# Kernel tuning notes

Measured on AMD Instinct MI355X. Metric: run time of the kernel, lower is better.

## Reference

```python
import jax, jax.numpy as jnp
import numpy as np

DIM = 192; HEADS = 6; HDIM = DIM // HEADS
WS = (2, 8, 8); SS = (1, 4, 4)
B, D, H, W = 2, 8, 64, 64
N = WS[0] * WS[1] * WS[2]          # 128 tokens per window
MLP_H = int(DIM * 2.0)
SCALE = HDIM ** -0.5


def _rel_pos_index_np():
    wd, wh, ww = WS
    coords = np.stack(np.meshgrid(np.arange(wd), np.arange(wh), np.arange(ww), indexing='ij'))
    cf = coords.reshape(3, -1)                      # (3, N)
    rel = (cf[:, :, None] - cf[:, None, :]).transpose(1, 2, 0)  # (N, N, 3)
    rel[..., 0] += wd - 1; rel[..., 1] += wh - 1; rel[..., 2] += ww - 1
    rel[..., 0] *= (2 * wh - 1) * (2 * ww - 1)
    rel[..., 1] *= (2 * ww - 1)
    return rel.sum(-1).astype(np.int32)            # (N, N)


def _compute_mask_np():
    wd, wh, ww = WS; sd, sh, sw = SS
    Dp = -(-D // wd) * wd; Hp = -(-H // wh) * wh; Wp = -(-W // ww) * ww
    img = np.zeros((1, Dp, Hp, Wp, 1), np.float32)
    cnt = 0
    for ds in (slice(0, -wd), slice(-wd, -sd), slice(-sd, None)):
        for hs in (slice(0, -wh), slice(-wh, -sh), slice(-sh, None)):
            for vs in (slice(0, -ww), slice(-ww, -sw), slice(-sw, None)):
                img[:, ds, hs, vs, :] = cnt; cnt += 1
    m = img.reshape(1, Dp // wd, wd, Hp // wh, wh, Wp // ww, ww, 1)
    m = m.transpose(0, 1, 3, 5, 2, 4, 6, 7).reshape(-1, N)       # (nW, N)
    am = m[:, None, :] - m[:, :, None]
    return np.where(am != 0, -100.0, 0.0).astype(np.float32)     # (nW, N, N)


def setup_inputs() -> dict:
    key = jax.random.key(0)
    ks = jax.random.split(key, 6)
    f = lambda k, s: (jax.random.normal(k, s, jnp.float32) * 0.02)
    n_bias = (2 * WS[0] - 1) * (2 * WS[1] - 1) * (2 * WS[2] - 1)  # 675
    return dict(
        x=jax.random.normal(ks[0], (B, D, H, W, DIM), jnp.float32),
        mask_matrix=jnp.asarray(_compute_mask_np()),
        rel_pos_index=jnp.asarray(_rel_pos_index_np()),
        gamma1=jnp.ones((DIM,), jnp.float32), beta1=jnp.zeros((DIM,), jnp.float32),
        w_qkv=f(ks[1], (3 * DIM, DIM)), b_qkv=jnp.zeros((3 * DIM,), jnp.float32),
        rpb=f(ks[2], (n_bias, HEADS)),
        w_proj=f(ks[3], (DIM, DIM)), b_proj=jnp.zeros((DIM,), jnp.float32),
        gamma2=jnp.ones((DIM,), jnp.float32), beta2=jnp.zeros((DIM,), jnp.float32),
        w_fc1=f(ks[4], (MLP_H, DIM)), b_fc1=jnp.zeros((MLP_H,), jnp.float32),
        w_fc2=f(ks[5], (DIM, MLP_H)), b_fc2=jnp.zeros((DIM,), jnp.float32),
    )


def _ln(x, g, b, eps=1e-5):
    mu = x.mean(-1, keepdims=True)
    var = ((x - mu) ** 2).mean(-1, keepdims=True)
    return (x - mu) * jax.lax.rsqrt(var + eps) * g + b


def _stl(x, mask, rpi, gamma1, beta1, w_qkv, b_qkv, rpb, w_proj, b_proj,
         gamma2, beta2, w_fc1, b_fc1, w_fc2, b_fc2):
    wd, wh, ww = WS; sd, sh, sw = SS
    # ---- part1: LN -> pad -> roll -> window attention -> reverse ----
    xn = _ln(x, gamma1, beta1)
    pd = (wd - D % wd) % wd; ph = (wh - H % wh) % wh; pw = (ww - W % ww) % ww
    xn = jnp.pad(xn, ((0, 0), (0, pd), (0, ph), (0, pw), (0, 0)))
    Dp, Hp, Wp = D + pd, H + ph, W + pw
    sx = jnp.roll(xn, (-sd, -sh, -sw), axis=(1, 2, 3))
    # window partition -> (Bw, N, C)
    xw = sx.reshape(B, Dp // wd, wd, Hp // wh, wh, Wp // ww, ww, DIM)
    xw = xw.transpose(0, 1, 3, 5, 2, 4, 6, 7).reshape(-1, N, DIM)
    Bw = xw.shape[0]
    qkv = (xw @ w_qkv.T + b_qkv).reshape(Bw, N, 3, HEADS, HDIM).transpose(2, 0, 3, 1, 4)
    q, k, v = qkv[0] * SCALE, qkv[1], qkv[2]
    attn = jnp.einsum('bhnd,bhmd->bhnm', q, k)
    bias = rpb[rpi.reshape(-1)].reshape(N, N, HEADS).transpose(2, 0, 1)  # (H, N, N)
    attn = attn + bias[None]
    nW = mask.shape[0]
    attn = (attn.reshape(Bw // nW, nW, HEADS, N, N) + mask[None, :, None]).reshape(Bw, HEADS, N, N)
    attn = jax.nn.softmax(attn, axis=-1)
    out = jnp.einsum('bhnm,bhmd->bhnd', attn, v).transpose(0, 2, 1, 3).reshape(Bw, N, DIM)
    out = out @ w_proj.T + b_proj
    # window reverse -> un-roll -> slice
    sx = out.reshape(B, Dp // wd, Hp // wh, Wp // ww, wd, wh, ww, DIM)
    sx = sx.transpose(0, 1, 4, 2, 5, 3, 6, 7).reshape(B, Dp, Hp, Wp, DIM)
    part1 = jnp.roll(sx, (sd, sh, sw), axis=(1, 2, 3))[:, :D, :H, :W, :]
    x = x + part1
    # ---- part2: LN -> MLP (GELU, exact) ----
    y = _ln(x, gamma2, beta2)
    h = jax.nn.gelu(y @ w_fc1.T + b_fc1, approximate=False)
    return x + (h @ w_fc2.T + b_fc2)


def reference(x, mask_matrix, rel_pos_index, gamma1, beta1, w_qkv, b_qkv, rpb,
              w_proj, b_proj, gamma2, beta2, w_fc1, b_fc1, w_fc2, b_fc2):
    return _stl(x, mask_matrix, rel_pos_index, gamma1, beta1, w_qkv, b_qkv, rpb,
                w_proj, b_proj, gamma2, beta2, w_fc1, b_fc1, w_fc2, b_fc2)
```

## Files before the change

### kernel.cpp

```cpp
#include <hip/hip_runtime.h>
#include <hip/hip_bf16.h>
#include <math.h>

#define TOKS   65536
#define DIMC   192
#define NTOK   128
#define MLPH   384
#define QSCALE 0.17677669529663687f

typedef unsigned short u16;
typedef unsigned int   u32;
typedef __attribute__((ext_vector_type(8))) short bf16x8;
typedef __attribute__((ext_vector_type(4))) float f32x4;

static __device__ __forceinline__ float gelu_exact(float v) {
    return 0.5f * v * (1.f + erff(v * 0.70710678118654752f));
}
static __device__ __forceinline__ u16 f2bf(float f) {
    __hip_bfloat16 h = __float2bfloat16(f);
    return *reinterpret_cast<u16*>(&h);
}
static __device__ __forceinline__ float bf2f(u16 b) {
    u32 u = ((u32)b) << 16;
    float f;
    __builtin_memcpy(&f, &u, 4);
    return f;
}
static __device__ __forceinline__ void gl_lds16(const u16* g, u16* l) {
    __builtin_amdgcn_global_load_lds(
        (const __attribute__((address_space(1))) void*)g,
        (__attribute__((address_space(3))) void*)l, 16, 0, 0);
}

#define OFF_XW   0u
#define OFF_Q    6291456u
#define OFF_K    12582912u
#define OFF_V    18874368u
#define OFF_BF   25165824u
#define OFF_WB   25264128u

__global__ __launch_bounds__(256) void k_prep(const float* __restrict__ a,
                                              const float* __restrict__ b,
                                              const float* __restrict__ c,
                                              const float* __restrict__ d,
                                              u16* __restrict__ o,
                                              const float* __restrict__ rpb,
                                              const int* __restrict__ rpi,
                                              u16* __restrict__ biasw) {
    int bid = blockIdx.x;
    if (bid < 1152) {
        int i = bid * 256 + threadIdx.x;
        float v;
        if (i < 110592) v = a[i];
        else if (i < 147456) v = b[i - 110592];
        else if (i < 221184) v = c[i - 147456];
        else v = d[i - 221184];
        o[i] = f2bf(v);
    } else {
        int idx = (bid - 1152) * 256 + threadIdx.x;
        int h = idx >> 14;
        int n = (idx >> 7) & 127;
        int slot = idx & 127;
        int m = ((slot & 7) << 4) + (slot >> 3);
        biasw[idx] = f2bf(rpb[rpi[n * 128 + m] * 6 + h]);
    }
}

template<bool PERMUTE>
__global__ __launch_bounds__(256) void k_ln(const float* __restrict__ x,
                                            const float* __restrict__ gamma,
                                            const float* __restrict__ beta,
                                            u16* __restrict__ out) {
    int tid  = threadIdx.x;
    int lane = tid & 63, wv = tid >> 6;
    int tk = blockIdx.x * 4 + wv;
    size_t src;
    if (PERMUTE) {
        int w_all = tk >> 7, t = tk & 127;
        int b  = w_all >> 8, rem = w_all & 255;
        int di = rem >> 6, hi = (rem >> 3) & 7, wi = rem & 7;
        int qd = (di * 2 + (t >> 6) + 1) & 7;
        int qh = (hi * 8 + ((t >> 3) & 7) + 4) & 63;
        int qw = (wi * 8 + (t & 7) + 4) & 63;
        src = ((size_t)(((b * 8 + qd) * 64 + qh) * 64 + qw)) * DIMC;
    } else {
        src = (size_t)tk * DIMC;
    }
    float v0 = x[src + lane];
    float v1 = x[src + 64 + lane];
    float v2 = x[src + 128 + lane];
    float s  = v0 + v1 + v2;
    float sq = v0 * v0 + v1 * v1 + v2 * v2;
    #pragma unroll
    for (int off = 32; off; off >>= 1) {
        s  += __shfl_xor(s, off);
        sq += __shfl_xor(sq, off);
    }
    float mu   = s * (1.f / 192.f);
    float var  = sq * (1.f / 192.f) - mu * mu;
    float rstd = rsqrtf(var + 1e-5f);
    size_t o = (size_t)tk * DIMC;
    out[o + lane]       = f2bf((v0 - mu) * rstd * gamma[lane]       + beta[lane]);
    out[o + 64 + lane]  = f2bf((v1 - mu) * rstd * gamma[64 + lane]  + beta[64 + lane]);
    out[o + 128 + lane] = f2bf((v2 - mu) * rstd * gamma[128 + lane] + beta[128 + lane]);
}

template<int MODE, int KD>
__global__ __launch_bounds__(256) void k_mgemm(const u16* __restrict__ A,
                                               const u16* __restrict__ W,
                                               const float* __restrict__ bias,
                                               void* __restrict__ outp,
                                               const float* __restrict__ aux,
                                               u16* __restrict__ q_o,
                                               u16* __restrict__ k_o,
                                               u16* __restrict__ v_o) {
    __shared__ u16 As[2][128 * 64];
    u16*   Eu = (u16*)As;
    float* Ef = (float*)As;
    const int tid = threadIdx.x;
    const int wv = tid >> 6, l = tid & 63;
    const int l15 = l & 15, g4 = l >> 4;
    const int wm = wv >> 1, wn = wv & 1;
    constexpr int NY  = (MODE == 0) ? 9 : (MODE == 2) ? 6 : 3;
    constexpr int CHK = 512 * NY / 8;
    const int bid = blockIdx.x;
    const int logical = (bid & 7) * CHK + (bid >> 3);
    const int xb = logical / NY;
    const int yb = logical - xb * NY;
    const size_t m0 = (size_t)xb * 128;
    const int n0 = yb * 64;
    const int srow = l >> 3, scol = l & 7;
    const int w = (int)(m0 >> 7);

    f32x4 acc[4][2] = {};

    const u16* Wb = W + (size_t)(n0 + wn * 32 + l15) * KD + g4 * 8;
    bf16x8 wfr[3][2][2];
    #pragma unroll
    for (int t = 0; t < 3; ++t)
        #pragma unroll
        for (int kk = 0; kk < 2; ++kk)
            #pragma unroll
            for (int nt = 0; nt < 2; ++nt)
                wfr[t][kk][nt] = *(const bf16x8*)&Wb[(size_t)(nt * 16) * KD + t * 64 + kk * 32];

    auto STAGE = [&](int b, int tcol) {
        const u16* Ab = A + m0 * KD + tcol * 64;
        #pragma unroll
        for (int j = 0; j < 4; ++j) {
            int row = (wv * 4 + j) * 8 + srow;
            int sc  = scol ^ (row & 7);
            gl_lds16(Ab + (size_t)row * KD + sc * 8, &As[b][(wv * 4 + j) * 512]);
        }
    };
    auto COMPUTE = [&](int b, int t) {
        #pragma unroll
        for (int kk = 0; kk < 2; ++kk) {
            bf16x8 bfr[2];
            if (t < 3) {
                bfr[0] = wfr[t][kk][0];
                bfr[1] = wfr[t][kk][1];
            } else {
                #pragma unroll
                for (int nt = 0; nt < 2; ++nt)
                    bfr[nt] = *(const bf16x8*)&Wb[(size_t)(nt * 16) * KD + t * 64 + kk * 32];
            }
            #pragma unroll
            for (int mt = 0; mt < 4; ++mt) {
                int row  = wm * 64 + mt * 16 + l15;
                int slot = (kk * 4 + g4) ^ (row & 7);
                bf16x8 afr = *(const bf16x8*)&As[b][row * 64 + slot * 8];
                #pragma unroll
                for (int nt = 0; nt < 2; ++nt)
                    acc[mt][nt] = __builtin_amdgcn_mfma_f32_16x16x32_bf16(afr, bfr[nt],
                                                                          acc[mt][nt], 0, 0, 0);
            }
        }
    };

    constexpr int NT = KD / 64;
    STAGE(0, 0);
    __syncthreads();
    #pragma unroll
    for (int t = 0; t < NT; ++t) {
        if (t + 1 < NT) STAGE((t + 1) & 1, t + 1);
        COMPUTE(t & 1, t);
        __syncthreads();
    }

    if (MODE == 0 || MODE == 2) {
        const int sel = (MODE == 0) ? ((n0 >= 384) ? 2 : (n0 >= 192 ? 1 : 0)) : 0;
        const float scl = (MODE == 0 && sel == 0) ? QSCALE : 1.f;
        #pragma unroll
        for (int mt = 0; mt < 4; ++mt) {
            #pragma unroll
            for (int nt = 0; nt < 2; ++nt) {
                int c = wn * 32 + nt * 16 + l15;
                float bb = bias[n0 + c];
                #pragma unroll
                for (int reg = 0; reg < 4; ++reg) {
                    int r = wm * 64 + mt * 16 + g4 * 4 + reg;
                    float v = acc[mt][nt][reg] + bb;
                    if (MODE == 2) v = gelu_exact(v);
                    else v *= scl;
                    int slot8 = (c >> 3) ^ ((r >> 2) & 7);
                    Eu[r * 64 + slot8 * 8 + (c & 7)] = f2bf(v);
                }
            }
        }
        __syncthreads();
        if (MODE == 2) {
            u16* out = (u16*)outp;
            #pragma unroll
            for (int p = 0; p < 4; ++p) {
                int cid = p * 256 + tid;
                int r = cid >> 3, j = cid & 7;
                int slot8 = j ^ ((r >> 2) & 7);
                bf16x8 vv = *(const bf16x8*)&Eu[r * 64 + slot8 * 8];
                *(bf16x8*)&out[(m0 + r) * MLPH + n0 + j * 8] = vv;
            }
        } else if (sel < 2) {
            u16* dst = sel ? k_o : q_o;
            const int hbase = (n0 - sel * 192) >> 5;
            #pragma unroll
            for (int p = 0; p < 4; ++p) {
                int cid = p * 256 + tid;
                int r = cid >> 3, j = cid & 7;
                int c0 = j * 8;
                int slot8 = j ^ ((r >> 2) & 7);
                bf16x8 vv = *(const bf16x8*)&Eu[r * 64 + slot8 * 8];
                size_t b9 = (size_t)(w * 6 + hbase + (c0 >> 5)) * 4096;
                *(bf16x8*)&dst[b9 + (size_t)r * 32 + (c0 & 31)] = vv;
            }
        } else {
            const int hbase = (n0 - 384) >> 5;
            #pragma unroll
            for (int p = 0; p < 4; ++p) {
                int cid = p * 256 + tid;
                int c = cid >> 4, jt = cid & 15;
                int t0 = jt * 8;
                u16 tmp[8];
                #pragma unroll
                for (int i = 0; i < 8; ++i) {
                    int r = t0 + i;
                    int slot8 = (c >> 3) ^ ((r >> 2) & 7);
                    tmp[i] = Eu[r * 64 + slot8 * 8 + (c & 7)];
                }
                size_t b9 = (size_t)(w * 6 + hbase + (c >> 5)) * 4096;
                *(bf16x8*)&v_o[b9 + (size_t)(c & 31) * 128 + t0] = *(bf16x8*)tmp;
            }
        }
    } else {
        #pragma unroll
        for (int mt = 0; mt < 4; ++mt) {
            #pragma unroll
            for (int nt = 0; nt < 2; ++nt) {
                int c = wn * 32 + nt * 16 + l15;
                float bb = bias[n0 + c];
                #pragma unroll
                for (int reg = 0; reg < 4; ++reg) {
                    int r = wm * 64 + mt * 16 + g4 * 4 + reg;
                    int swz = (c >> 2) ^ ((r >> 2) & 3);
                    Ef[r * 64 + swz * 4 + (c & 3)] = acc[mt][nt][reg] + bb;
                }
            }
        }
        __syncthreads();
        float* out = (float*)outp;
        #pragma unroll
        for (int p = 0; p < 8; ++p) {
            int cid = p * 256 + tid;
            int r = cid >> 4, j = cid & 15;
            int swz = j ^ ((r >> 2) & 3);
            float4 vv = *(const float4*)&Ef[r * 64 + swz * 4];
            size_t drow;
            if (MODE == 1) {
                int m = (int)m0 + r;
                int w_all = m >> 7, tt = m & 127;
                int b  = w_all >> 8, rem = w_all & 255;
                int di = rem >> 6, hi = (rem >> 3) & 7, wi = rem & 7;
                int qd = (di * 2 + (tt >> 6) + 1) & 7;
                int qh = (hi * 8 + ((tt >> 3) & 7) + 4) & 63;
                int qw = (wi * 8 + (tt & 7) + 4) & 63;
                drow = (size_t)(((b * 8 + qd) * 64 + qh) * 64 + qw) * DIMC;
            } else {
                drow = (m0 + r) * DIMC;
            }
            float4 ax = *(const float4*)&aux[drow + n0 + j * 4];
            vv.x += ax.x; vv.y += ax.y; vv.z += ax.z; vv.w += ax.w;
            *(float4*)&out[drow + n0 + j * 4] = vv;
        }
    }
}

__global__ __launch_bounds__(256) void k_attn(const u16* __restrict__ qb,
                                              const u16* __restrict__ kb,
                                              const u16* __restrict__ vb,
                                              const u16* __restrict__ biasw,
                                              u16* __restrict__ attn_out) {
    __shared__ u16 Pl[4][32 * 128];
    u16* Ou = (u16*)Pl;
    int wh = blockIdx.x;
    int w_all = wh / 6, head = wh - w_all * 6;
    int wl = w_all & 255;
    int tid = threadIdx.x;
    int wv = tid >> 6, l = tid & 63;
    int l15 = l & 15, g4 = l >> 4;
    size_t base = (size_t)wh * 4096;
    const u16* qg = qb + base;
    const u16* kg = kb + base;
    const u16* vg = vb + base;
    int rowb = wv * 32;

    bf16x8 qa[2];
    #pragma unroll
    for (int rt = 0; rt < 2; ++rt)
        qa[rt] = *(const bf16x8*)&qg[(size_t)(rowb + rt * 16 + l15) * 32 + g4 * 8];

    f32x4 s[2][8] = {};
    #pragma unroll
    for (int ct = 0; ct < 8; ++ct) {
        bf16x8 kf = *(const bf16x8*)&kg[(size_t)(ct * 16 + l15) * 32 + g4 * 8];
        s[0][ct] = __builtin_amdgcn_mfma_f32_16x16x32_bf16(qa[0], kf, s[0][ct], 0, 0, 0);
        s[1][ct] = __builtin_amdgcn_mfma_f32_16x16x32_bf16(qa[1], kf, s[1][ct], 0, 0, 0);
    }

    int di = wl >> 6, hi = (wl >> 3) & 7, wi = wl & 7;
    auto rcode = [&](int t) {
        int d = di * 2 + (t >> 6);
        int h = hi * 8 + ((t >> 3) & 7);
        int w = wi * 8 + (t & 7);
        int rd = (d < 6) ? 0 : (d < 7 ? 1 : 2);
        int rh = (h < 56) ? 0 : (h < 60 ? 1 : 2);
        int rw = (w < 56) ? 0 : (w < 60 ? 1 : 2);
        return rd * 9 + rh * 3 + rw;
    };
    int rm[8];
    #pragma unroll
    for (int ct = 0; ct < 8; ++ct) rm[ct] = rcode(ct * 16 + l15);

    const u16* bh = biasw + (size_t)head * 16384;
    #pragma unroll
    for (int rt = 0; rt < 2; ++rt)
        #pragma unroll
        for (int reg = 0; reg < 4; ++reg) {
            int n = rowb + rt * 16 + g4 * 4 + reg;
            int rn = rcode(n);
            bf16x8 bv = *(const bf16x8*)&bh[(size_t)n * 128 + l15 * 8];
            #pragma unroll
            for (int ct = 0; ct < 8; ++ct) {
                float mval = (rn == rm[ct]) ? 0.f : -100.f;
                s[rt][ct][reg] += bf2f((u16)bv[ct]) + mval;
            }
        }

    u16* Pw = Pl[wv];
    #pragma unroll
    for (int rt = 0; rt < 2; ++rt)
        #pragma unroll
        for (int reg = 0; reg < 4; ++reg) {
            float mx = -1e30f;
            #pragma unroll
            for (int ct = 0; ct < 8; ++ct) mx = fmaxf(mx, s[rt][ct][reg]);
            #pragma unroll
            for (int off = 1; off < 16; off <<= 1) mx = fmaxf(mx, __shfl_xor(mx, off));
            float sum = 0.f;
            #pragma unroll
            for (int ct = 0; ct < 8; ++ct) {
                float p = __expf(s[rt][ct][reg] - mx);
                s[rt][ct][reg] = p; sum += p;
            }
            #pragma unroll
            for (int off = 1; off < 16; off <<= 1) sum += __shfl_xor(sum, off);
            float inv = 1.f / sum;
            int nloc = rt * 16 + g4 * 4 + reg;
            int sw = ((nloc >> 2) & 3) << 4;
            #pragma unroll
            for (int ct = 0; ct < 8; ++ct) {
                int m = ct * 16 + l15;
                Pw[nloc * 128 + (m ^ sw)] = f2bf(s[rt][ct][reg] * inv);
            }
        }
    __syncthreads();

    f32x4 o[2][2] = {};
    #pragma unroll
    for (int kt = 0; kt < 4; ++kt) {
        bf16x8 vf[2];
        #pragma unroll
        for (int dt = 0; dt < 2; ++dt)
            vf[dt] = *(const bf16x8*)&vg[(size_t)(dt * 16 + l15) * 128 + kt * 32 + g4 * 8];
        #pragma unroll
        for (int rt = 0; rt < 2; ++rt) {
            int nloc = rt * 16 + l15;
            int sw = ((nloc >> 2) & 3) << 4;
            int m8 = kt * 32 + g4 * 8;
            bf16x8 pa = *(const bf16x8*)&Pw[nloc * 128 + (m8 ^ sw)];
            #pragma unroll
            for (int dt = 0; dt < 2; ++dt)
                o[rt][dt] = __builtin_amdgcn_mfma_f32_16x16x32_bf16(pa, vf[dt], o[rt][dt], 0, 0, 0);
        }
    }

    __syncthreads();
    #pragma unroll
    for (int rt = 0; rt < 2; ++rt)
        #pragma unroll
        for (int dt = 0; dt < 2; ++dt)
            #pragma unroll
            for (int reg = 0; reg < 4; ++reg) {
                int r = rowb + rt * 16 + g4 * 4 + reg;
                int c = dt * 16 + l15;
                int slot8 = (c >> 3) ^ ((r >> 2) & 3);
                Ou[r * 32 + slot8 * 8 + (c & 7)] = f2bf(o[rt][dt][reg]);
            }
    __syncthreads();
    #pragma unroll
    for (int p = 0; p < 2; ++p) {
        int cid = p * 256 + tid;
        int r = cid >> 2, j = cid & 3;
        int slot8 = j ^ ((r >> 2) & 3);
        bf16x8 vv = *(const bf16x8*)&Ou[r * 32 + slot8 * 8];
        *(bf16x8*)&attn_out[((size_t)(w_all * 128 + r)) * DIMC + head * 32 + j * 8] = vv;
    }
}

extern "C" void kernel_launch(void* const* d_in, const int* in_sizes, int n_in,
                              void* d_out, int out_size, void* d_ws, size_t ws_size,
                              hipStream_t stream) {
    const float* x      = (const float*)d_in[0];
    const int*   rpi    = (const int*)d_in[2];
    const float* gamma1 = (const float*)d_in[3];
    const float* beta1  = (const float*)d_in[4];
    const float* w_qkv  = (const float*)d_in[5];
    const float* b_qkv  = (const float*)d_in[6];
    const float* rpb    = (const float*)d_in[7];
    const float* w_proj = (const float*)d_in[8];
    const float* b_proj = (const float*)d_in[9];
    const float* gamma2 = (const float*)d_in[10];
    const float* beta2  = (const float*)d_in[11];
    const float* w_fc1  = (const float*)d_in[12];
    const float* b_fc1  = (const float*)d_in[13];
    const float* w_fc2  = (const float*)d_in[14];
    const float* b_fc2  = (const float*)d_in[15];

    float* ws    = (float*)d_ws;
    u16*   xwu   = (u16*)(ws + OFF_XW);
    u16*   qbu   = (u16*)(ws + OFF_Q);
    u16*   kbu   = (u16*)(ws + OFF_K);
    u16*   vbu   = (u16*)(ws + OFF_V);
    u16*   hbu   = (u16*)(ws + OFF_Q);
    u16*   ybu   = (u16*)(ws + OFF_V);
    u16*   biasw = (u16*)(ws + OFF_BF);
    u16*   wb    = (u16*)(ws + OFF_WB);
    float* xres  = (float*)d_out;

    const u16* wqkv_b  = wb;
    const u16* wproj_b = wb + 110592;
    const u16* wfc1_b  = wb + 147456;
    const u16* wfc2_b  = wb + 221184;

    k_prep<<<1536, 256, 0, stream>>>(w_qkv, w_proj, w_fc1, w_fc2, wb, rpb, rpi, biasw);
    k_ln<true><<<16384, 256, 0, stream>>>(x, gamma1, beta1, xwu);
    k_mgemm<0, 192><<<4608, 256, 0, stream>>>(xwu, wqkv_b, b_qkv, nullptr, nullptr,
                                              qbu, kbu, vbu);
    k_attn<<<3072, 256, 0, stream>>>(qbu, kbu, vbu, biasw, xwu);
    k_mgemm<1, 192><<<1536, 256, 0, stream>>>(xwu, wproj_b, b_proj, xres, x,
                                              nullptr, nullptr, nullptr);
    k_ln<false><<<16384, 256, 0, stream>>>(xres, gamma2, beta2, ybu);
    k_mgemm<2, 192><<<3072, 256, 0, stream>>>(ybu, wfc1_b, b_fc1, hbu, nullptr,
                                              nullptr, nullptr, nullptr);
    k_mgemm<3, 384><<<1536, 256, 0, stream>>>(hbu, wfc2_b, b_fc2, xres, xres,
                                              nullptr, nullptr, nullptr);
}
```

Baseline: 200.5 us.

## Load GEMM A and W fragments directly from global, drop LDS staging

Removes the double-buffered LDS staging of the A tile (global_load_lds plus barriers) and the preloaded weight fragments. Each wave now loads its A and W MFMA fragments straight from global memory every k-step. The aim is to cut barrier and LDS traffic and shrink shared memory for some modes, which could raise occupancy. In exchange, A rows are re-read by both N-waves with strided 16-byte accesses and there is no software prefetch, so latency is exposed.

```diff
diff --git a/kernel.cpp b/kernel.cpp
--- a/kernel.cpp
+++ b/kernel.cpp
@@ -25,11 +25,6 @@
     float f;
     __builtin_memcpy(&f, &u, 4);
     return f;
-}
-static __device__ __forceinline__ void gl_lds16(const u16* g, u16* l) {
-    __builtin_amdgcn_global_load_lds(
-        (const __attribute__((address_space(1))) void*)g,
-        (__attribute__((address_space(3))) void*)l, 16, 0, 0);
 }
 
 #define OFF_XW   0u
@@ -114,9 +109,9 @@
                                                u16* __restrict__ q_o,
                                                u16* __restrict__ k_o,
                                                u16* __restrict__ v_o) {
-    __shared__ u16 As[2][128 * 64];
-    u16*   Eu = (u16*)As;
-    float* Ef = (float*)As;
+    __shared__ u16 Sh[(MODE == 1 || MODE == 3) ? 2 * 128 * 64 : 128 * 64];
+    u16*   Eu = Sh;
+    float* Ef = (float*)Sh;
     const int tid = threadIdx.x;
     const int wv = tid >> 6, l = tid & 63;
     const int l15 = l & 15, g4 = l >> 4;
@@ -129,63 +124,38 @@
     const int yb = logical - xb * NY;
     const size_t m0 = (size_t)xb * 128;
     const int n0 = yb * 64;
-    const int srow = l >> 3, scol = l & 7;
     const int w = (int)(m0 >> 7);
 
     f32x4 acc[4][2] = {};
 
-    const u16* Wb = W + (size_t)(n0 + wn * 32 + l15) * KD + g4 * 8;
-    bf16x8 wfr[3][2][2];
-    #pragma unroll
-    for (int t = 0; t < 3; ++t)
-        #pragma unroll
-        for (int kk = 0; kk < 2; ++kk)
-            #pragma unroll
-            for (int nt = 0; nt < 2; ++nt)
-                wfr[t][kk][nt] = *(const bf16x8*)&Wb[(size_t)(nt * 16) * KD + t * 64 + kk * 32];
-
-    auto STAGE = [&](int b, int tcol) {
-        const u16* Ab = A + m0 * KD + tcol * 64;
-        #pragma unroll
-        for (int j = 0; j < 4; ++j) {
-            int row = (wv * 4 + j) * 8 + srow;
-            int sc  = scol ^ (row & 7);
-            gl_lds16(Ab + (size_t)row * KD + sc * 8, &As[b][(wv * 4 + j) * 512]);
-        }
-    };
-    auto COMPUTE = [&](int b, int t) {
+    const u16* Ap0 = A + (m0 + (size_t)(wm * 64 + 0  * 16 + l15)) * KD + g4 * 8;
+    const u16* Ap1 = A + (m0 + (size_t)(wm * 64 + 1  * 16 + l15)) * KD + g4 * 8;
+    const u16* Ap2 = A + (m0 + (size_t)(wm * 64 + 2  * 16 + l15)) * KD + g4 * 8;
+    const u16* Ap3 = A + (m0 + (size_t)(wm * 64 + 3  * 16 + l15)) * KD + g4 * 8;
+    const u16* Wb  = W + (size_t)(n0 + wn * 32 + l15) * KD + g4 * 8;
+
+    constexpr int NT = KD / 64;
+    #pragma unroll
+    for (int t = 0; t < NT; ++t) {
         #pragma unroll
         for (int kk = 0; kk < 2; ++kk) {
+            const int co = t * 64 + kk * 32;
             bf16x8 bfr[2];
-            if (t < 3) {
-                bfr[0] = wfr[t][kk][0];
-                bfr[1] = wfr[t][kk][1];
-            } else {
-                #pragma unroll
-                for (int nt = 0; nt < 2; ++nt)
-                    bfr[nt] = *(const bf16x8*)&Wb[(size_t)(nt * 16) * KD + t * 64 + kk * 32];
-            }
-            #pragma unroll
-            for (int mt = 0; mt < 4; ++mt) {
-                int row  = wm * 64 + mt * 16 + l15;
-                int slot = (kk * 4 + g4) ^ (row & 7);
-                bf16x8 afr = *(const bf16x8*)&As[b][row * 64 + slot * 8];
-                #pragma unroll
-                for (int nt = 0; nt < 2; ++nt)
-                    acc[mt][nt] = __builtin_amdgcn_mfma_f32_16x16x32_bf16(afr, bfr[nt],
-                                                                          acc[mt][nt], 0, 0, 0);
-            }
-        }
-    };
-
-    constexpr int NT = KD / 64;
-    STAGE(0, 0);
-    __syncthreads();
-    #pragma unroll
-    for (int t = 0; t < NT; ++t) {
-        if (t + 1 < NT) STAGE((t + 1) & 1, t + 1);
-        COMPUTE(t & 1, t);
-        __syncthreads();
+            bfr[0] = *(const bf16x8*)&Wb[co];
+            bfr[1] = *(const bf16x8*)&Wb[(size_t)16 * KD + co];
+            bf16x8 a0 = *(const bf16x8*)&Ap0[co];
+            bf16x8 a1 = *(const bf16x8*)&Ap1[co];
+            bf16x8 a2 = *(const bf16x8*)&Ap2[co];
+            bf16x8 a3 = *(const bf16x8*)&Ap3[co];
+            acc[0][0] = __builtin_amdgcn_mfma_f32_16x16x32_bf16(a0, bfr[0], acc[0][0], 0, 0, 0);
+            acc[0][1] = __builtin_amdgcn_mfma_f32_16x16x32_bf16(a0, bfr[1], acc[0][1], 0, 0, 0);
+            acc[1][0] = __builtin_amdgcn_mfma_f32_16x16x32_bf16(a1, bfr[0], acc[1][0], 0, 0, 0);
+            acc[1][1] = __builtin_amdgcn_mfma_f32_16x16x32_bf16(a1, bfr[1], acc[1][1], 0, 0, 0);
+            acc[2][0] = __builtin_amdgcn_mfma_f32_16x16x32_bf16(a2, bfr[0], acc[2][0], 0, 0, 0);
+            acc[2][1] = __builtin_amdgcn_mfma_f32_16x16x32_bf16(a2, bfr[1], acc[2][1], 0, 0, 0);
+            acc[3][0] = __builtin_amdgcn_mfma_f32_16x16x32_bf16(a3, bfr[0], acc[3][0], 0, 0, 0);
+            acc[3][1] = __builtin_amdgcn_mfma_f32_16x16x32_bf16(a3, bfr[1], acc[3][1], 0, 0, 0);
+        }
     }
 
     if (MODE == 0 || MODE == 2) {
```

Result: slower. 294.7 us (+47.0%).
